# Kernel tuning notes

Hardware: AMD Instinct MI355X
Metric: run time of the kernel (lower is better)

The kernel has to match this reference:

```python
import jax, jax.numpy as jnp
import numpy as np

MAX_REL = 8  # max_relative_position
B, H, L, D = 2, 16, 2048, 64


def setup_inputs() -> dict:
    key = jax.random.key(0)
    kq, kk, kv, kb = jax.random.split(key, 4)
    return {
        "q": jax.random.normal(kq, (B, H, L, D), dtype=jnp.float32),
        "k": jax.random.normal(kk, (B, H, L, D), dtype=jnp.float32),
        "v": jax.random.normal(kv, (B, H, L, D), dtype=jnp.float32),
        "relative_bias": jax.random.normal(kb, (2 * MAX_REL + 1,), dtype=jnp.float32),
    }


def reference(q, k, v, relative_bias):
    Bq, Hq, Lq, Dq = q.shape
    scale = jnp.sqrt(jnp.asarray(Dq, dtype=q.dtype))
    # [B,H,L,L] attention scores
    scores = jnp.einsum("bhqd,bhkd->bhqk", q, k) / scale
    pos = jnp.arange(Lq)
    rel = pos[None, :] - pos[:, None]                 # [L,L] (col - row), matches torch code
    idx = jnp.clip(rel, -MAX_REL, MAX_REL) + MAX_REL  # [L,L] in [0, 2*MAX_REL]
    bias = relative_bias[idx]                         # [L,L] gather from bias table
    scores = scores + bias[None, None, :, :]
    attn = jax.nn.softmax(scores, axis=-1)
    return jnp.einsum("bhqk,bhkd->bhqd", attn, v)
```

## Files before the change

kernel.cpp:

```cpp
#include <hip/hip_runtime.h>
#include <hip/hip_bf16.h>


#define LOG2E 1.44269504088896f

constexpr int Lv = 2048, Dv = 64;
constexpr int BH  = 32;
constexpr int BQ  = 128;
constexpr int BKT = 64;
constexpr int NQT = Lv / BQ;
constexpr int NKT = Lv / BKT;
constexpr int LDK = 72;
constexpr int LDO = 68;
constexpr int MAXREL = 8;

typedef __bf16 bf16x8 __attribute__((ext_vector_type(8)));
typedef __bf16 bf16x4 __attribute__((ext_vector_type(4)));
typedef float  f32x4  __attribute__((ext_vector_type(4)));

static __device__ __forceinline__ unsigned pack2bf(float a, float b) {
    __bf16 x = (__bf16)a, y = (__bf16)b;
    unsigned short ux = __builtin_bit_cast(unsigned short, x);
    unsigned short uy = __builtin_bit_cast(unsigned short, y);
    return (unsigned)ux | ((unsigned)uy << 16);
}

__global__
__attribute__((amdgpu_flat_work_group_size(512, 512), amdgpu_waves_per_eu(4, 4)))
void relattn_kernel(
    const float* __restrict__ Q, const float* __restrict__ K,
    const float* __restrict__ V, const float* __restrict__ RB,
    float* __restrict__ O)
{
    constexpr int SKBYTES  = 2 * BKT * LDK * 2;
    constexpr int SVBYTES  = 2 * Dv  * LDK * 2;
    constexpr int PADBYTES = 20480;
    __shared__ __align__(16) unsigned char smem[SKBYTES + SVBYTES + PADBYTES];
    __shared__ float sRB[2 * MAXREL + 1];
    __bf16* sK = (__bf16*)smem;
    __bf16* sV = (__bf16*)(smem + SKBYTES);

    const int tid  = threadIdx.x;
    const int w    = tid >> 6;
    const int lane = tid & 63;
    const int l16  = lane & 15;
    const int lg   = lane >> 4;
    const int pair = w >> 1;
    const int wh   = w & 1;

    const int bh = blockIdx.x & (BH - 1);
    const int qt = blockIdx.x >> 5;

    const size_t base = (size_t)bh * Lv * Dv;
    const float* Qb = Q + base + (size_t)qt * BQ * Dv;
    const float* Kb = K + base;
    const float* Vb = V + base;
    float*       Ob = O + base + (size_t)qt * BQ * Dv;

    if (tid < 2 * MAXREL + 1) sRB[tid] = RB[tid] * LOG2E;

    const float qsc = 0.125f * LOG2E;
    bf16x8 qfrag[2][2];
    #pragma unroll
    for (int h = 0; h < 2; ++h) {
        const float* qrow = Qb + (pair * 32 + h * 16 + l16) * Dv;
        #pragma unroll
        for (int s = 0; s < 2; ++s) {
            const float4 a = *(const float4*)(qrow + lg * 8 + 32 * s);
            const float4 b = *(const float4*)(qrow + lg * 8 + 32 * s + 4);
            bf16x8 f;
            f[0] = (__bf16)(a.x * qsc); f[1] = (__bf16)(a.y * qsc);
            f[2] = (__bf16)(a.z * qsc); f[3] = (__bf16)(a.w * qsc);
            f[4] = (__bf16)(b.x * qsc); f[5] = (__bf16)(b.y * qsc);
            f[6] = (__bf16)(b.z * qsc); f[7] = (__bf16)(b.w * qsc);
            qfrag[h][s] = f;
        }
    }

    bf16x8 ones;
    #pragma unroll
    for (int j = 0; j < 8; ++j) ones[j] = (__bf16)1.0f;

    f32x4 oacc[2][4];
    f32x4 lfrag[2];
    #pragma unroll
    for (int h = 0; h < 2; ++h) {
        #pragma unroll
        for (int r = 0; r < 4; ++r) lfrag[h][r] = 0.f;
        #pragma unroll
        for (int t = 0; t < 4; ++t)
            #pragma unroll
            for (int r = 0; r < 4; ++r) oacc[h][t][r] = 0.f;
    }

    const int kr0 = tid >> 4;
    const int kc4 = (tid & 15) * 4;
    const int vkk0 = (tid & 31) * 2;
    const int vd0  = (tid >> 5) * 4;
    const int vcol = (vkk0 & 35) | ((vkk0 & 12) << 1) | ((vkk0 & 16) >> 2);

    float4 kreg[2], vreg[2];
    bf16x4   kpk[2];
    unsigned vpk[4];

    auto loadKV = [&](int kt) {
        const float* Ks = Kb + (size_t)kt * BKT * Dv;
        const float* Vs = Vb + (size_t)kt * BKT * Dv;
        kreg[0] = *(const float4*)(Ks + kr0 * Dv + kc4);
        kreg[1] = *(const float4*)(Ks + (32 + kr0) * Dv + kc4);
        vreg[0] = *(const float4*)(Vs + vkk0 * Dv + vd0);
        vreg[1] = *(const float4*)(Vs + (vkk0 + 1) * Dv + vd0);
    };
    auto convKV = [&]() {
        #pragma unroll
        for (int p = 0; p < 2; ++p) {
            bf16x4 pk;
            pk[0] = (__bf16)kreg[p].x; pk[1] = (__bf16)kreg[p].y;
            pk[2] = (__bf16)kreg[p].z; pk[3] = (__bf16)kreg[p].w;
            kpk[p] = pk;
        }
        #pragma unroll
        for (int j = 0; j < 4; ++j)
            vpk[j] = pack2bf(vreg[0][j], vreg[1][j]);
    };

    loadKV(0);
    convKV();

    const int qw0 = qt * BQ + pair * 32;
    const int qgl = qw0 + l16;

    for (int kt = 0; kt < NKT; ++kt) {
        const int buf = kt & 1;
        __bf16* sKb = sK + buf * (BKT * LDK);
        __bf16* sVb = sV + buf * (Dv * LDK);

        *(bf16x4*)&sKb[kr0 * LDK + kc4]          = kpk[0];
        *(bf16x4*)&sKb[(32 + kr0) * LDK + kc4]   = kpk[1];
        #pragma unroll
        for (int j = 0; j < 4; ++j)
            *(unsigned*)&sVb[(vd0 + j) * LDK + vcol] = vpk[j];
        if (kt + 1 < NKT) loadKV(kt + 1);
        __syncthreads();

        const int k0 = kt * BKT + wh * 32;
        f32x4 sacc[2][2];
        #pragma unroll
        for (int h = 0; h < 2; ++h) {
            const int qlo = qw0 + h * 16;
            if (k0 >= qlo + 15 + MAXREL) {
                const float bc = sRB[2 * MAXREL];
                #pragma unroll
                for (int tl = 0; tl < 2; ++tl)
                    #pragma unroll
                    for (int r = 0; r < 4; ++r) sacc[h][tl][r] = bc;
            } else if (k0 + 31 + MAXREL <= qlo) {
                const float bc = sRB[0];
                #pragma unroll
                for (int tl = 0; tl < 2; ++tl)
                    #pragma unroll
                    for (int r = 0; r < 4; ++r) sacc[h][tl][r] = bc;
            } else {
                const int kkb = k0 + lg * 4 - (qgl + h * 16);
                #pragma unroll
                for (int tl = 0; tl < 2; ++tl) {
                    #pragma unroll
                    for (int r = 0; r < 4; ++r) {
                        int d = kkb + tl * 16 + r;
                        d = d < -MAXREL ? -MAXREL : (d > MAXREL ? MAXREL : d);
                        sacc[h][tl][r] = sRB[d + MAXREL];
                    }
                }
            }
        }

        #pragma unroll
        for (int s = 0; s < 2; ++s) {
            #pragma unroll
            for (int tl = 0; tl < 2; ++tl) {
                bf16x8 a = *(const bf16x8*)&sKb[((2 * wh + tl) * 16 + l16) * LDK + lg * 8 + 32 * s];
                sacc[0][tl] = __builtin_amdgcn_mfma_f32_16x16x32_bf16(a, qfrag[0][s], sacc[0][tl], 0, 0, 0);
                sacc[1][tl] = __builtin_amdgcn_mfma_f32_16x16x32_bf16(a, qfrag[1][s], sacc[1][tl], 0, 0, 0);
            }
        }

        if (kt + 1 < NKT) convKV();

        bf16x8 pfrag[2];
        #pragma unroll
        for (int h = 0; h < 2; ++h)
            #pragma unroll
            for (int tl = 0; tl < 2; ++tl)
                #pragma unroll
                for (int r = 0; r < 4; ++r)
                    pfrag[h][tl * 4 + r] =
                        (__bf16)__builtin_amdgcn_exp2f(sacc[h][tl][r]);

        lfrag[0] = __builtin_amdgcn_mfma_f32_16x16x32_bf16(ones, pfrag[0], lfrag[0], 0, 0, 0);
        lfrag[1] = __builtin_amdgcn_mfma_f32_16x16x32_bf16(ones, pfrag[1], lfrag[1], 0, 0, 0);

        #pragma unroll
        for (int t = 0; t < 4; ++t) {
            bf16x8 vf = *(const bf16x8*)&sVb[(t * 16 + l16) * LDK + lg * 8 + 32 * wh];
            oacc[0][t] = __builtin_amdgcn_mfma_f32_16x16x32_bf16(vf, pfrag[0], oacc[0][t], 0, 0, 0);
            oacc[1][t] = __builtin_amdgcn_mfma_f32_16x16x32_bf16(vf, pfrag[1], oacc[1][t], 0, 0, 0);
        }
    }

    float lh[2];
    lh[0] = lfrag[0][0];
    lh[1] = lfrag[1][0];

    __syncthreads();
    float* sO = (float*)smem;
    float* sL = (float*)(smem + 4 * 32 * LDO * 4);
    if (wh == 1) {
        #pragma unroll
        for (int h = 0; h < 2; ++h) {
            #pragma unroll
            for (int t = 0; t < 4; ++t)
                *(f32x4*)&sO[(pair * 32 + h * 16 + l16) * LDO + t * 16 + lg * 4] = oacc[h][t];
            if (lg == 0) sL[pair * 32 + h * 16 + l16] = lh[h];
        }
    }
    __syncthreads();
    if (wh == 0) {
        #pragma unroll
        for (int h = 0; h < 2; ++h) {
            const float lt = lh[h] + sL[pair * 32 + h * 16 + l16];
            const float linv = 1.f / lt;
            float* orow = Ob + (pair * 32 + h * 16 + l16) * Dv;
            #pragma unroll
            for (int t = 0; t < 4; ++t) {
                f32x4 oo = *(const f32x4*)&sO[(pair * 32 + h * 16 + l16) * LDO + t * 16 + lg * 4];
                float4 o;
                o.x = (oacc[h][t][0] + oo[0]) * linv;
                o.y = (oacc[h][t][1] + oo[1]) * linv;
                o.z = (oacc[h][t][2] + oo[2]) * linv;
                o.w = (oacc[h][t][3] + oo[3]) * linv;
                *(float4*)(orow + t * 16 + lg * 4) = o;
            }
        }
    }
}

extern "C" void kernel_launch(void* const* d_in, const int* in_sizes, int n_in,
                              void* d_out, int out_size, void* d_ws, size_t ws_size,
                              hipStream_t stream) {
    const float* q  = (const float*)d_in[0];
    const float* k  = (const float*)d_in[1];
    const float* v  = (const float*)d_in[2];
    const float* rb = (const float*)d_in[3];
    float* out = (float*)d_out;
    relattn_kernel<<<dim3(BH * NQT), dim3(512), 0, stream>>>(q, k, v, rb, out);
}
```

Measured before the change: 136.9 us.

## Quad-buffer K/V tiles in LDS and sync once per pair of tiles

Replaces the double-buffered K/V LDS staging, which needed a barrier every tile, with four K and four V buffers in dynamic shared memory. Two tiles are processed per barrier while the next pair is prefetched and written into the other buffers. The global-to-LDS write is moved after the exp2 stage so it overlaps with the MFMA work. This halves the number of block-wide barriers and lengthens load latency hiding, but raises LDS use to about 72KB per block and adds register pressure.

After: 140.1 us. +2.3%, slower.

```diff
diff --git a/kernel.cpp b/kernel.cpp
--- a/kernel.cpp
+++ b/kernel.cpp
@@ -14,6 +14,12 @@
 constexpr int LDO = 68;
 constexpr int MAXREL = 8;
 
+constexpr int TILEB   = BKT * LDK * 2;
+constexpr int KOFF    = 0;
+constexpr int VOFF    = 4 * TILEB;
+constexpr int RBOFF   = 8 * TILEB;
+constexpr int DYNLDS  = RBOFF + 128;
+
 typedef __bf16 bf16x8 __attribute__((ext_vector_type(8)));
 typedef __bf16 bf16x4 __attribute__((ext_vector_type(4)));
 typedef float  f32x4  __attribute__((ext_vector_type(4)));
@@ -32,13 +38,8 @@
     const float* __restrict__ V, const float* __restrict__ RB,
     float* __restrict__ O)
 {
-    constexpr int SKBYTES  = 2 * BKT * LDK * 2;
-    constexpr int SVBYTES  = 2 * Dv  * LDK * 2;
-    constexpr int PADBYTES = 20480;
-    __shared__ __align__(16) unsigned char smem[SKBYTES + SVBYTES + PADBYTES];
-    __shared__ float sRB[2 * MAXREL + 1];
-    __bf16* sK = (__bf16*)smem;
-    __bf16* sV = (__bf16*)(smem + SKBYTES);
+    extern __shared__ __align__(16) unsigned char smem[];
+    float* sRB = (float*)(smem + RBOFF);
 
     const int tid  = threadIdx.x;
     const int w    = tid >> 6;
@@ -100,8 +101,6 @@
     const int vcol = (vkk0 & 35) | ((vkk0 & 12) << 1) | ((vkk0 & 16) >> 2);
 
     float4 kreg[2], vreg[2];
-    bf16x4   kpk[2];
-    unsigned vpk[4];
 
     auto loadKV = [&](int kt) {
         const float* Ks = Kb + (size_t)kt * BKT * Dv;
@@ -111,37 +110,29 @@
         vreg[0] = *(const float4*)(Vs + vkk0 * Dv + vd0);
         vreg[1] = *(const float4*)(Vs + (vkk0 + 1) * Dv + vd0);
     };
-    auto convKV = [&]() {
+    auto stageKV = [&](int buf) {
+        __bf16* sKb = (__bf16*)(smem + KOFF + buf * TILEB);
+        __bf16* sVb = (__bf16*)(smem + VOFF + buf * TILEB);
         #pragma unroll
         for (int p = 0; p < 2; ++p) {
             bf16x4 pk;
             pk[0] = (__bf16)kreg[p].x; pk[1] = (__bf16)kreg[p].y;
             pk[2] = (__bf16)kreg[p].z; pk[3] = (__bf16)kreg[p].w;
-            kpk[p] = pk;
+            *(bf16x4*)&sKb[(p * 32 + kr0) * LDK + kc4] = pk;
         }
         #pragma unroll
         for (int j = 0; j < 4; ++j)
-            vpk[j] = pack2bf(vreg[0][j], vreg[1][j]);
+            *(unsigned*)&sVb[(vd0 + j) * LDK + vcol] =
+                pack2bf(vreg[0][j], vreg[1][j]);
     };
-
-    loadKV(0);
-    convKV();
 
     const int qw0 = qt * BQ + pair * 32;
     const int qgl = qw0 + l16;
 
-    for (int kt = 0; kt < NKT; ++kt) {
-        const int buf = kt & 1;
-        __bf16* sKb = sK + buf * (BKT * LDK);
-        __bf16* sVb = sV + buf * (Dv * LDK);
-
-        *(bf16x4*)&sKb[kr0 * LDK + kc4]          = kpk[0];
-        *(bf16x4*)&sKb[(32 + kr0) * LDK + kc4]   = kpk[1];
-        #pragma unroll
-        for (int j = 0; j < 4; ++j)
-            *(unsigned*)&sVb[(vd0 + j) * LDK + vcol] = vpk[j];
-        if (kt + 1 < NKT) loadKV(kt + 1);
-        __syncthreads();
+    auto TILE = [&](int kt, int rbuf, int wbuf, int pf) {
+        if (pf < NKT) loadKV(pf);
+        __bf16* sKr = (__bf16*)(smem + KOFF + rbuf * TILEB);
+        __bf16* sVr = (__bf16*)(smem + VOFF + rbuf * TILEB);
 
         const int k0 = kt * BKT + wh * 32;
         f32x4 sacc[2][2];
@@ -178,14 +169,12 @@
         for (int s = 0; s < 2; ++s) {
             #pragma unroll
             for (int tl = 0; tl < 2; ++tl) {
-                bf16x8 a = *(const bf16x8*)&sKb[((2 * wh + tl) * 16 + l16) * LDK + lg * 8 + 32 * s];
+                bf16x8 a = *(const bf16x8*)&sKr[((2 * wh + tl) * 16 + l16) * LDK + lg * 8 + 32 * s];
                 sacc[0][tl] = __builtin_amdgcn_mfma_f32_16x16x32_bf16(a, qfrag[0][s], sacc[0][tl], 0, 0, 0);
                 sacc[1][tl] = __builtin_amdgcn_mfma_f32_16x16x32_bf16(a, qfrag[1][s], sacc[1][tl], 0, 0, 0);
             }
         }
 
-        if (kt + 1 < NKT) convKV();
-
         bf16x8 pfrag[2];
         #pragma unroll
         for (int h = 0; h < 2; ++h)
@@ -196,22 +185,35 @@
                     pfrag[h][tl * 4 + r] =
                         (__bf16)__builtin_amdgcn_exp2f(sacc[h][tl][r]);
 
+        if (pf < NKT) stageKV(wbuf);
+
         lfrag[0] = __builtin_amdgcn_mfma_f32_16x16x32_bf16(ones, pfrag[0], lfrag[0], 0, 0, 0);
         lfrag[1] = __builtin_amdgcn_mfma_f32_16x16x32_bf16(ones, pfrag[1], lfrag[1], 0, 0, 0);
 
         #pragma unroll
         for (int t = 0; t < 4; ++t) {
-            bf16x8 vf = *(const bf16x8*)&sVb[(t * 16 + l16) * LDK + lg * 8 + 32 * wh];
+            bf16x8 vf = *(const bf16x8*)&sVr[(t * 16 + l16) * LDK + lg * 8 + 32 * wh];
             oacc[0][t] = __builtin_amdgcn_mfma_f32_16x16x32_bf16(vf, pfrag[0], oacc[0][t], 0, 0, 0);
             oacc[1][t] = __builtin_amdgcn_mfma_f32_16x16x32_bf16(vf, pfrag[1], oacc[1][t], 0, 0, 0);
         }
+    };
+
+    loadKV(0); stageKV(0);
+    loadKV(1); stageKV(1);
+    __syncthreads();
+
+    for (int g = 0; g < NKT / 2; ++g) {
+        const int rp = (g & 1) << 1;
+        const int wp = ((g + 1) & 1) << 1;
+        TILE(2 * g,     rp,     wp,     2 * g + 2);
+        TILE(2 * g + 1, rp + 1, wp + 1, 2 * g + 3);
+        __syncthreads();
     }
 
     float lh[2];
     lh[0] = lfrag[0][0];
     lh[1] = lfrag[1][0];
 
-    __syncthreads();
     float* sO = (float*)smem;
     float* sL = (float*)(smem + 4 * 32 * LDO * 4);
     if (wh == 1) {
@@ -252,5 +254,11 @@
     const float* v  = (const float*)d_in[2];
     const float* rb = (const float*)d_in[3];
     float* out = (float*)d_out;
-    relattn_kernel<<<dim3(BH * NQT), dim3(512), 0, stream>>>(q, k, v, rb, out);
+    static bool attr_set = false;
+    if (!attr_set) {
+        hipFuncSetAttribute((const void*)relattn_kernel,
+                            hipFuncAttributeMaxDynamicSharedMemorySize, DYNLDS);
+        attr_set = true;
+    }
+    relattn_kernel<<<dim3(BH * NQT), dim3(512), DYNLDS, stream>>>(q, k, v, rb, out);
 }
```
